# Performance work log

Hardware: AMD Instinct MI355X
Metric: run time of the kernel (lower is better)

Reference implementation:

```python
import jax, jax.numpy as jnp
import numpy as np

HEADS = 8
DIM_HEAD = 64
SCALE = DIM_HEAD ** -0.5
POS_DIM = 64


def _sincos_pe(H, W, dim, dtype):
    # matches build_2d_sincos_pos_embed: [1, dim, H, W]
    y = jnp.linspace(-1.0, 1.0, H)[:, None] * jnp.ones((1, W), jnp.float32)
    x = jnp.ones((H, 1), jnp.float32) * jnp.linspace(-1.0, 1.0, W)[None, :]
    omega = 1.0 / (10000.0 ** (jnp.arange(dim // 4, dtype=jnp.float32) / (dim // 4)))
    px = x[..., None] * omega  # [H, W, dim//4]
    py = y[..., None] * omega
    pe = jnp.concatenate([jnp.sin(px), jnp.cos(px), jnp.sin(py), jnp.cos(py)], axis=-1)
    return pe.transpose(2, 0, 1)[None].astype(dtype)


def _conv2d(x, w):
    return jax.lax.conv_general_dilated(
        x, w, (1, 1), 'SAME', dimension_numbers=('NCHW', 'OIHW', 'NCHW'))


def _sobel(d):
    kx = jnp.array([[1, 0, -1], [2, 0, -2], [1, 0, -1]], jnp.float32).reshape(1, 1, 3, 3)
    ky = jnp.array([[1, 2, 1], [0, 0, 0], [-1, -2, -1]], jnp.float32).reshape(1, 1, 3, 3)
    return _conv2d(d, kx), _conv2d(d, ky)


def setup_inputs() -> dict:
    key = jax.random.key(0)
    ks = jax.random.split(key, 8)
    B, C, H, W = 2, 256, 64, 64
    hid = HEADS * DIM_HEAD  # 512
    s = 0.02
    return {
        'x': jax.random.normal(ks[0], (B, C, H, W), jnp.float32),
        'dsm': jax.random.uniform(ks[1], (B, 1, H, W), jnp.float32),
        'wq': jax.random.normal(ks[2], (hid, C), jnp.float32) * s,
        'wkv': jax.random.normal(ks[3], (2 * hid, C + 1), jnp.float32) * s,
        'wout': jax.random.normal(ks[4], (C, hid), jnp.float32) * s,
        'bout': jnp.zeros((C,), jnp.float32),
        'w_hape': jax.random.normal(ks[5], (hid, POS_DIM + 3), jnp.float32) * s,
        'b_hape': jnp.zeros((hid,), jnp.float32),
        'w_alpha': jax.random.normal(ks[6], (1, 1, 3, 3), jnp.float32) * 0.1,
        'b_alpha': jnp.zeros((1,), jnp.float32),
    }


def reference(x, dsm, wq, wkv, wout, bout, w_hape, b_hape, w_alpha, b_alpha):
    B, C, H, W = x.shape
    hid = wq.shape[0]
    # per-sample min-max normalize DSM over spatial dims
    dmin = dsm.min(axis=(2, 3), keepdims=True)
    dmax = dsm.max(axis=(2, 3), keepdims=True)
    d = (dsm - dmin) / (dmax - dmin + 1e-6)
    # HAPE: [PE | h | grad_h] -> 1x1 conv to hidden
    pe = jnp.broadcast_to(_sincos_pe(H, W, POS_DIM, x.dtype), (B, POS_DIM, H, W))
    gx, gy = _sobel(d)
    hape_in = jnp.concatenate([pe, d, gx, gy], axis=1)  # [B, 67, H, W]
    hape_k = jnp.einsum('oc,bchw->bohw', w_hape, hape_in) + b_hape[None, :, None, None]
    # QKV via 1x1 convs
    q = jnp.einsum('oc,bchw->bohw', wq, x)
    kv = jnp.einsum('oc,bchw->bohw', wkv, jnp.concatenate([x, d], axis=1))
    k = kv[:, :hid] + hape_k
    v = kv[:, hid:]
    to_heads = lambda t: t.reshape(B, HEADS, DIM_HEAD, H * W)  # b (h c) x y -> b h c (xy)
    qh = to_heads(q) * SCALE
    kh = to_heads(k)
    vh = to_heads(v)
    sim = jnp.einsum('bhdi,bhdj->bhij', qh, kh)  # [B, h, N, N]
    attn = jax.nn.softmax(sim, axis=-1)
    out = jnp.einsum('bhij,bhdj->bhid', attn, vh)  # [B, h, N, d]
    # b h (x y) d -> b (h d) x y
    out = out.transpose(0, 1, 3, 2).reshape(B, HEADS * DIM_HEAD, H, W)
    out = jnp.einsum('oc,bchw->bohw', wout, out) + bout[None, :, None, None]
    # fine: gradient-magnitude alpha gating
    mag = jnp.sqrt(jnp.maximum(gx, 0.0) ** 2 + jnp.maximum(gy, 0.0) ** 2 + 1e-12)
    alpha = jax.nn.sigmoid(_conv2d(mag, w_alpha) + b_alpha[None, :, None, None])
    return x + out * alpha
```

## Files before the change

### kernel.cpp

```cpp
#include <hip/hip_runtime.h>
#include <math.h>

#define NPOS 4096
#define MTOT 8192
#define KP   352
#define HT 64
#define WT 64

typedef unsigned short ushortT;
typedef short v8s __attribute__((ext_vector_type(8)));
typedef float v4f __attribute__((ext_vector_type(4)));

static __device__ __forceinline__ ushortT bfr(float f) {
    union { float f; unsigned u; } v; v.f = f;
    return (ushortT)((v.u + 0x8000u) >> 16);
}
static __device__ __forceinline__ unsigned pack2bf(float a, float b) {
    union { float f; unsigned u; } ua, ub; ua.f = a; ub.f = b;
    return __builtin_amdgcn_perm(ub.u + 0x8000u, ua.u + 0x8000u, 0x07060302u);
}
static __device__ __forceinline__ unsigned pack2bf_t(float a, float b) {
    union { float f; unsigned u; } ua, ub; ua.f = a; ub.f = b;
    return __builtin_amdgcn_perm(ub.u, ua.u, 0x07060302u);
}
static __device__ __forceinline__ float fexp2(float x) {
#if __has_builtin(__builtin_amdgcn_exp2f)
    return __builtin_amdgcn_exp2f(x);
#else
    return exp2f(x);
#endif
}

__global__ void k_minmax(const float* __restrict__ dsm, float* __restrict__ mm) {
    int b = blockIdx.x;
    const float* p = dsm + (size_t)b * NPOS;
    float mn = 1e30f, mx = -1e30f;
    for (int i = threadIdx.x; i < NPOS; i += 256) {
        float v = p[i];
        mn = fminf(mn, v); mx = fmaxf(mx, v);
    }
    for (int off = 32; off; off >>= 1) {
        mn = fminf(mn, __shfl_xor(mn, off, 64));
        mx = fmaxf(mx, __shfl_xor(mx, off, 64));
    }
    __shared__ float smn[4], smx[4];
    int wid = threadIdx.x >> 6;
    if ((threadIdx.x & 63) == 0) { smn[wid] = mn; smx[wid] = mx; }
    __syncthreads();
    if (threadIdx.x == 0) {
        mn = fminf(fminf(smn[0], smn[1]), fminf(smn[2], smn[3]));
        mx = fmaxf(fmaxf(smx[0], smx[1]), fmaxf(smx[2], smx[3]));
        mm[b * 2 + 0] = mn; mm[b * 2 + 1] = mx;
    }
}

__global__ void k_prep(const float* __restrict__ dsm, const float* __restrict__ mm,
                       const float* __restrict__ walpha, const float* __restrict__ balpha,
                       ushortT* __restrict__ F, float* __restrict__ alpha) {
    int idx = blockIdx.x * 256 + threadIdx.x;
    int b = idx / NPOS, n = idx % NPOS;
    int hh = n / WT, ww = n % WT;
    float dmin = mm[b * 2], dmax = mm[b * 2 + 1];
    float inv = 1.0f / (dmax - dmin + 1e-6f);
    const float* dp = dsm + (size_t)b * NPOS;

    float dwin[5][5];
    #pragma unroll
    for (int dy = 0; dy < 5; dy++)
        #pragma unroll
        for (int dx = 0; dx < 5; dx++) {
            int y = hh + dy - 2, x = ww + dx - 2;
            float v = 0.0f;
            if (y >= 0 && y < HT && x >= 0 && x < WT) v = (dp[y * WT + x] - dmin) * inv;
            dwin[dy][dx] = v;
        }

    float gxc = 0.f, gyc = 0.f;
    float conv = 0.f;
    #pragma unroll
    for (int oy = 0; oy < 3; oy++)
        #pragma unroll
        for (int ox = 0; ox < 3; ox++) {
            int qy = hh + oy - 1, qx = ww + ox - 1;
            float m = 0.0f;
            if (qy >= 0 && qy < HT && qx >= 0 && qx < WT) {
                float gx = dwin[oy][ox] - dwin[oy][ox + 2]
                         + 2.f * dwin[oy + 1][ox] - 2.f * dwin[oy + 1][ox + 2]
                         + dwin[oy + 2][ox] - dwin[oy + 2][ox + 2];
                float gy = dwin[oy][ox] + 2.f * dwin[oy][ox + 1] + dwin[oy][ox + 2]
                         - dwin[oy + 2][ox] - 2.f * dwin[oy + 2][ox + 1] - dwin[oy + 2][ox + 2];
                if (oy == 1 && ox == 1) { gxc = gx; gyc = gy; }
                float rx = fmaxf(gx, 0.f), ry = fmaxf(gy, 0.f);
                m = sqrtf(rx * rx + ry * ry + 1e-12f);
            }
            conv += walpha[oy * 3 + ox] * m;
        }
    alpha[idx] = 1.f / (1.f + __expf(-(conv + balpha[0])));

    ushortT* fb = F + (size_t)idx * KP;
    fb[256] = bfr(dwin[2][2]);
    fb[257] = bfr(gxc);
    fb[258] = bfr(gyc);
    float xc = -1.f + 2.f * (float)ww / 63.f;
    float yc = -1.f + 2.f * (float)hh / 63.f;
    const float l2w = 13.287712379549449f;
    #pragma unroll
    for (int i = 0; i < 16; i++) {
        float omega = exp2f(-(float)i * (l2w / 16.f));
        float px = xc * omega, py = yc * omega;
        fb[259 + i]      = bfr(__sinf(px));
        fb[259 + 16 + i] = bfr(__cosf(px));
        fb[259 + 32 + i] = bfr(__sinf(py));
        fb[259 + 48 + i] = bfr(__cosf(py));
    }
    #pragma unroll
    for (int z = 323; z < KP; z++) fb[z] = 0;
}

__global__ void k_cast(const float* __restrict__ x, ushortT* __restrict__ F) {
    __shared__ __align__(16) ushortT Tl[64][72];
    int nt = blockIdx.x * 64;
    int b = blockIdx.y >> 2, ct = (blockIdx.y & 3) * 64;
    int t = threadIdx.x;
    #pragma unroll
    for (int rep = 0; rep < 4; rep++) {
        int row = rep * 16 + (t >> 4), c4 = (t & 15) * 4;
        float4 f4 = *(const float4*)&x[((size_t)(b * 256 + ct + row)) * NPOS + nt + c4];
        Tl[c4 + 0][row] = bfr(f4.x);
        Tl[c4 + 1][row] = bfr(f4.y);
        Tl[c4 + 2][row] = bfr(f4.z);
        Tl[c4 + 3][row] = bfr(f4.w);
    }
    __syncthreads();
    #pragma unroll
    for (int rep = 0; rep < 2; rep++) {
        int slot = rep * 256 + t, row = slot >> 3, c8 = slot & 7;
        *(uint4*)&F[((size_t)(b * 4096 + nt + row)) * KP + ct + c8 * 8] = *(uint4*)&Tl[row][c8 * 8];
    }
}

__global__ void k_wcprep(const float* __restrict__ wq, const float* __restrict__ wkv,
                         const float* __restrict__ whape, const float* __restrict__ bhape,
                         ushortT* __restrict__ Wc, float* __restrict__ biasc) {
    int idx = blockIdx.x * 256 + threadIdx.x;
    int o = idx / KP, k = idx % KP;
    float v = 0.f;
    if (o < 512) {
        if (k < 256) v = wq[o * 256 + k] * 0.18033688011112042f;
        if (k == 0) biasc[o] = 0.f;
    } else if (o < 1024) {
        int r = o - 512;
        if (k < 257) v = wkv[r * 257 + k];
        if (k == 256)      v += whape[r * 67 + 64];
        else if (k == 257) v = whape[r * 67 + 65];
        else if (k == 258) v = whape[r * 67 + 66];
        else if (k >= 259 && k < 323) v = whape[r * 67 + (k - 259)];
        if (k == 0) biasc[o] = bhape[r];
    } else {
        int r = o - 512;
        if (k < 257) v = wkv[r * 257 + k];
        if (k == 0) biasc[o] = 0.f;
    }
    Wc[idx] = bfr(v);
}

__global__ void k_wout(const float* __restrict__ wout, ushortT* __restrict__ woutb) {
    int idx = blockIdx.x * 256 + threadIdx.x;
    woutb[idx] = bfr(wout[idx]);
}

__global__ __launch_bounds__(256) void k_gemm1(const ushortT* __restrict__ Wc, const ushortT* __restrict__ F,
                                               const float* __restrict__ biasc,
                                               ushortT* __restrict__ qT, ushortT* __restrict__ kT,
                                               ushortT* __restrict__ vv) {
    __shared__ __align__(16) ushortT Al[64][40];
    __shared__ __align__(16) ushortT Bl[64][40];
    __shared__ __align__(16) ushortT Vt[64][72];
    int mt = blockIdx.x * 64;
    int ot = blockIdx.y * 64;
    int t = threadIdx.x, w = t >> 6, lane = t & 63, u = lane & 15, quad = lane >> 4;
    int arow = t >> 2, ac8 = t & 3;
    v4f acc[4] = {};
    for (int k0 = 0; k0 < KP; k0 += 32) {
        __syncthreads();
        *(uint4*)&Al[arow][ac8 * 8] = *(const uint4*)&Wc[(size_t)(ot + arow) * KP + k0 + ac8 * 8];
        *(uint4*)&Bl[arow][ac8 * 8] = *(const uint4*)&F[(size_t)(mt + arow) * KP + k0 + ac8 * 8];
        __syncthreads();
        v8s a = *(v8s*)&Al[w * 16 + u][quad * 8];
        #pragma unroll
        for (int n4 = 0; n4 < 4; n4++) {
            v8s bb = *(v8s*)&Bl[n4 * 16 + u][quad * 8];
            acc[n4] = __builtin_amdgcn_mfma_f32_16x16x32_bf16(a, bb, acc[n4], 0, 0, 0);
        }
    }
    int obase = ot + w * 16 + quad * 4;
    float bo[4];
    #pragma unroll
    for (int r = 0; r < 4; r++) bo[r] = biasc[obase + r];
    if (ot < 1024) {
        int h = (ot >> 6) & 7;
        ushortT* dst = (ot < 512) ? qT : kT;
        #pragma unroll
        for (int n4 = 0; n4 < 4; n4++) {
            int m = mt + n4 * 16 + u;
            uint2 val;
            val.x = pack2bf(acc[n4][0] + bo[0], acc[n4][1] + bo[1]);
            val.y = pack2bf(acc[n4][2] + bo[2], acc[n4][3] + bo[3]);
            *(uint2*)&dst[((size_t)h * MTOT + m) * 64 + w * 16 + quad * 4] = val;
        }
    } else {
        __syncthreads();
        #pragma unroll
        for (int n4 = 0; n4 < 4; n4++) {
            int ml = n4 * 16 + u;
            #pragma unroll
            for (int r = 0; r < 4; r++) Vt[w * 16 + quad * 4 + r][ml] = bfr(acc[n4][r] + bo[r]);
        }
        __syncthreads();
        #pragma unroll
        for (int rep = 0; rep < 2; rep++) {
            int slot = rep * 256 + t, row = slot >> 3, c8 = slot & 7;
            *(uint4*)&vv[(size_t)(ot - 1024 + row) * MTOT + mt + c8 * 8] = *(uint4*)&Vt[row][c8 * 8];
        }
    }
}

#define LIDX(row, cb) (((row) << 6) + ((((cb) ^ ((row) & 7))) << 3))
__global__ __launch_bounds__(256, 2) void k_flash(const ushortT* __restrict__ qT,
                                                  const ushortT* __restrict__ kT,
                                                  const ushortT* __restrict__ vv,
                                                  float* __restrict__ Opart,
                                                  float* __restrict__ liPart) {
    __shared__ __align__(16) ushortT Kbuf[2][64 * 64];
    __shared__ __align__(16) ushortT Vbuf[2][64 * 64];
    __shared__ __align__(16) ushortT Pw[4][64 * 64];

    int it = blockIdx.x;
    int bh = blockIdx.y;
    int half = blockIdx.z;
    int b = bh >> 3, h = bh & 7;
    int colbase = b * NPOS;
    int t = threadIdx.x, w = t >> 6, lane = t & 63, u = lane & 15, quad = lane >> 4;
    int qb = it * 256 + w * 64;

    const ushortT* Qg = qT + ((size_t)h * MTOT + colbase + qb) * 64;
    const ushortT* Kg = kT + ((size_t)h * MTOT + colbase + half * 2048) * 64;
    const ushortT* Vg = vv + ((size_t)(h * 64)) * MTOT + colbase + half * 2048;
    ushortT* P = &Pw[w][0];

    int row0 = t >> 3,        c80 = t & 7;
    int row1 = (256 + t) >> 3, c81 = t & 7;

    v8s bq[4][2];
    #pragma unroll
    for (int g = 0; g < 4; g++)
        #pragma unroll
        for (int hf = 0; hf < 2; hf++)
            bq[g][hf] = *(const v8s*)&Qg[(size_t)(g * 16 + u) * 64 + hf * 32 + quad * 8];

    float li[4] = {0.f, 0.f, 0.f, 0.f};
    v4f O[4][4] = {};

    uint4 kr0 = *(const uint4*)&Kg[(size_t)row0 * 64 + c80 * 8];
    uint4 kr1 = *(const uint4*)&Kg[(size_t)row1 * 64 + c81 * 8];
    uint4 vr0 = *(const uint4*)&Vg[(size_t)row0 * MTOT + c80 * 8];
    uint4 vr1 = *(const uint4*)&Vg[(size_t)row1 * MTOT + c81 * 8];

    for (int jc = 0; jc < 32; jc++) {
        int cur = jc & 1;
        *(uint4*)&Kbuf[cur][LIDX(row0, c80)] = kr0;
        *(uint4*)&Kbuf[cur][LIDX(row1, c81)] = kr1;
        *(uint4*)&Vbuf[cur][LIDX(row0, c80)] = vr0;
        *(uint4*)&Vbuf[cur][LIDX(row1, c81)] = vr1;
        if (jc + 1 < 32) {
            int jb = (jc + 1) * 64;
            kr0 = *(const uint4*)&Kg[(size_t)(jb + row0) * 64 + c80 * 8];
            kr1 = *(const uint4*)&Kg[(size_t)(jb + row1) * 64 + c81 * 8];
            vr0 = *(const uint4*)&Vg[(size_t)row0 * MTOT + jb + c80 * 8];
            vr1 = *(const uint4*)&Vg[(size_t)row1 * MTOT + jb + c81 * 8];
        }
        __syncthreads();

        const ushortT* Kb = &Kbuf[cur][0];
        const ushortT* Vb = &Vbuf[cur][0];

        #pragma unroll
        for (int k4 = 0; k4 < 4; k4++) {
            v8s ak0 = *(const v8s*)&Kb[LIDX(k4 * 16 + u, quad)];
            v8s ak1 = *(const v8s*)&Kb[LIDX(k4 * 16 + u, 4 + quad)];
            v4f st[4];
            #pragma unroll
            for (int g = 0; g < 4; g++) {
                st[g] = (v4f){0.f, 0.f, 0.f, 0.f};
                st[g] = __builtin_amdgcn_mfma_f32_16x16x32_bf16(ak0, bq[g][0], st[g], 0, 0, 0);
                st[g] = __builtin_amdgcn_mfma_f32_16x16x32_bf16(ak1, bq[g][1], st[g], 0, 0, 0);
            }
            #pragma unroll
            for (int g = 0; g < 4; g++) {
                float p0 = fexp2(st[g][0]);
                float p1 = fexp2(st[g][1]);
                float p2 = fexp2(st[g][2]);
                float p3 = fexp2(st[g][3]);
                li[g] += (p0 + p1) + (p2 + p3);
                uint2 pv; pv.x = pack2bf_t(p0, p1); pv.y = pack2bf_t(p2, p3);
                *(uint2*)&P[LIDX(g * 16 + u, k4 * 2 + (quad >> 1)) + (quad & 1) * 4] = pv;
            }
        }

        v8s bp[4][2];
        #pragma unroll
        for (int g = 0; g < 4; g++)
            #pragma unroll
            for (int ks = 0; ks < 2; ks++)
                bp[g][ks] = *(v8s*)&P[LIDX(g * 16 + u, ks * 4 + quad)];
        #pragma unroll
        for (int d4 = 0; d4 < 4; d4++) {
            v8s av0 = *(const v8s*)&Vb[LIDX(d4 * 16 + u, quad)];
            v8s av1 = *(const v8s*)&Vb[LIDX(d4 * 16 + u, 4 + quad)];
            #pragma unroll
            for (int g = 0; g < 4; g++) {
                O[d4][g] = __builtin_amdgcn_mfma_f32_16x16x32_bf16(av0, bp[g][0], O[d4][g], 0, 0, 0);
                O[d4][g] = __builtin_amdgcn_mfma_f32_16x16x32_bf16(av1, bp[g][1], O[d4][g], 0, 0, 0);
            }
        }
    }

    #pragma unroll
    for (int g = 0; g < 4; g++) {
        li[g] += __shfl_xor(li[g], 16, 64);
        li[g] += __shfl_xor(li[g], 32, 64);
        int q = qb + g * 16 + u;
        size_t m2 = (size_t)(half * 2 + b) * 4096 + q;
        size_t base = m2 * 512 + h * 64;
        #pragma unroll
        for (int d4 = 0; d4 < 4; d4++) {
            float4 o4;
            o4.x = O[d4][g][0]; o4.y = O[d4][g][1]; o4.z = O[d4][g][2]; o4.w = O[d4][g][3];
            *(float4*)&Opart[base + d4 * 16 + quad * 4] = o4;
        }
        if (quad == 0) liPart[m2 * 8 + h] = li[g];
    }
}

__global__ __launch_bounds__(256) void k_comb(const float* __restrict__ Opart,
                                              const float* __restrict__ liPart,
                                              ushortT* __restrict__ aoB) {
    int tid = blockIdx.x * 256 + threadIdx.x;
    int m = tid >> 7, c4 = (tid & 127) * 4, h = c4 >> 6;
    float l = liPart[(size_t)m * 8 + h] + liPart[(size_t)(8192 + m) * 8 + h];
    float inv = 1.f / l;
    float4 o0 = *(const float4*)&Opart[(size_t)m * 512 + c4];
    float4 o1 = *(const float4*)&Opart[(size_t)(8192 + m) * 512 + c4];
    uint2 val;
    val.x = pack2bf((o0.x + o1.x) * inv, (o0.y + o1.y) * inv);
    val.y = pack2bf((o0.z + o1.z) * inv, (o0.w + o1.w) * inv);
    *(uint2*)&aoB[(size_t)m * 512 + c4] = val;
}

__global__ __launch_bounds__(256) void k_gemm2(const ushortT* __restrict__ woutb, const ushortT* __restrict__ aoB,
                                               const float* __restrict__ bout, const float* __restrict__ x,
                                               const float* __restrict__ alpha, float* __restrict__ out) {
    __shared__ __align__(16) ushortT Al[64][40];
    __shared__ __align__(16) ushortT Bl[64][40];
    int mt = blockIdx.x * 64;
    int ot = blockIdx.y * 64;
    int t = threadIdx.x, w = t >> 6, lane = t & 63, u = lane & 15, quad = lane >> 4;
    int arow = t >> 2, ac8 = t & 3;
    v4f acc[4] = {};
    for (int k0 = 0; k0 < 512; k0 += 32) {
        __syncthreads();
        *(uint4*)&Al[arow][ac8 * 8] = *(const uint4*)&woutb[(size_t)(ot + arow) * 512 + k0 + ac8 * 8];
        *(uint4*)&Bl[arow][ac8 * 8] = *(const uint4*)&aoB[(size_t)(mt + arow) * 512 + k0 + ac8 * 8];
        __syncthreads();
        v8s a = *(v8s*)&Al[w * 16 + u][quad * 8];
        #pragma unroll
        for (int n4 = 0; n4 < 4; n4++) {
            v8s bb = *(v8s*)&Bl[n4 * 16 + u][quad * 8];
            acc[n4] = __builtin_amdgcn_mfma_f32_16x16x32_bf16(a, bb, acc[n4], 0, 0, 0);
        }
    }
    int b = mt >> 12, n0 = mt & 4095;
    int obase = ot + w * 16 + quad * 4;
    float bo[4];
    #pragma unroll
    for (int r = 0; r < 4; r++) bo[r] = bout[obase + r];
    #pragma unroll
    for (int n4 = 0; n4 < 4; n4++) {
        int n = n0 + n4 * 16 + u;
        float al = alpha[(size_t)b * NPOS + n];
        #pragma unroll
        for (int r = 0; r < 4; r++) {
            size_t xi = ((size_t)(b * 256 + obase + r)) * NPOS + n;
            out[xi] = x[xi] + (acc[n4][r] + bo[r]) * al;
        }
    }
}

extern "C" void kernel_launch(void* const* d_in, const int* in_sizes, int n_in,
                              void* d_out, int out_size, void* d_ws, size_t ws_size,
                              hipStream_t stream) {
    const float* x      = (const float*)d_in[0];
    const float* dsm    = (const float*)d_in[1];
    const float* wq     = (const float*)d_in[2];
    const float* wkv    = (const float*)d_in[3];
    const float* wout   = (const float*)d_in[4];
    const float* bout   = (const float*)d_in[5];
    const float* whape  = (const float*)d_in[6];
    const float* bhape  = (const float*)d_in[7];
    const float* walpha = (const float*)d_in[8];
    const float* balpha = (const float*)d_in[9];
    float* out = (float*)d_out;
    float* ws  = (float*)d_ws;

    size_t off = 0;
    float* mm    = ws + off; off += 256;
    float* alpha = ws + off; off += (size_t)2 * NPOS;
    float* biasc = ws + off; off += 2048;
    float* Opart  = ws + off; off += (size_t)2 * MTOT * 512;
    float* liPart = ws + off; off += (size_t)2 * MTOT * 8;
    ushortT* F     = (ushortT*)(ws + off); off += (size_t)MTOT * KP / 2;
    ushortT* Wc    = (ushortT*)(ws + off); off += (size_t)1536 * KP / 2;
    ushortT* woutb = (ushortT*)(ws + off); off += (size_t)256 * 512 / 2;
    ushortT* qT    = (ushortT*)(ws + off); off += (size_t)8 * MTOT * 64 / 2;
    ushortT* kT    = (ushortT*)(ws + off); off += (size_t)8 * MTOT * 64 / 2;
    ushortT* vv    = (ushortT*)(ws + off); off += (size_t)512 * MTOT / 2;
    ushortT* aoB   = (ushortT*)(ws + off); off += (size_t)MTOT * 512 / 2;
    (void)in_sizes; (void)n_in; (void)out_size; (void)ws_size;

    k_minmax<<<2, 256, 0, stream>>>(dsm, mm);
    k_prep<<<32, 256, 0, stream>>>(dsm, mm, walpha, balpha, F, alpha);
    k_cast<<<dim3(64, 8), 256, 0, stream>>>(x, F);
    k_wcprep<<<(1536 * KP) / 256, 256, 0, stream>>>(wq, wkv, whape, bhape, Wc, biasc);
    k_wout<<<512, 256, 0, stream>>>(wout, woutb);
    k_gemm1<<<dim3(128, 24), 256, 0, stream>>>(Wc, F, biasc, qT, kT, vv);
    k_flash<<<dim3(16, 16, 2), 256, 0, stream>>>(qT, kT, vv, Opart, liPart);
    k_comb<<<4096, 256, 0, stream>>>(Opart, liPart, aoB);
    k_gemm2<<<dim3(128, 4), 256, 0, stream>>>(woutb, aoB, bout, x, alpha, out);
}
```

Baseline: 212.8 us.

## Use direct global-to-LDS loads in flash, store bf16 partials, fuse combine into gemm2

```diff
diff --git a/kernel.cpp b/kernel.cpp
--- a/kernel.cpp
+++ b/kernel.cpp
@@ -22,6 +22,12 @@
 static __device__ __forceinline__ unsigned pack2bf_t(float a, float b) {
     union { float f; unsigned u; } ua, ub; ua.f = a; ub.f = b;
     return __builtin_amdgcn_perm(ub.u, ua.u, 0x07060302u);
+}
+static __device__ __forceinline__ float bf2f_lo(unsigned v) {
+    union { unsigned u; float f; } x; x.u = v << 16; return x.f;
+}
+static __device__ __forceinline__ float bf2f_hi(unsigned v) {
+    union { unsigned u; float f; } x; x.u = v & 0xffff0000u; return x.f;
 }
 static __device__ __forceinline__ float fexp2(float x) {
 #if __has_builtin(__builtin_amdgcn_exp2f)
@@ -29,6 +35,11 @@
 #else
     return exp2f(x);
 #endif
+}
+static __device__ __forceinline__ void ld_lds16(const ushortT* g, ushortT* l) {
+    __builtin_amdgcn_global_load_lds(
+        (const __attribute__((address_space(1))) unsigned int*)(const void*)g,
+        (__attribute__((address_space(3))) unsigned int*)(void*)l, 16, 0, 0);
 }
 
 __global__ void k_minmax(const float* __restrict__ dsm, float* __restrict__ mm) {
@@ -139,10 +150,18 @@
     }
 }
 
-__global__ void k_wcprep(const float* __restrict__ wq, const float* __restrict__ wkv,
-                         const float* __restrict__ whape, const float* __restrict__ bhape,
-                         ushortT* __restrict__ Wc, float* __restrict__ biasc) {
-    int idx = blockIdx.x * 256 + threadIdx.x;
+__global__ void k_wc(const float* __restrict__ wq, const float* __restrict__ wkv,
+                     const float* __restrict__ whape, const float* __restrict__ bhape,
+                     const float* __restrict__ wout,
+                     ushortT* __restrict__ Wc, float* __restrict__ biasc,
+                     ushortT* __restrict__ woutb) {
+    int bid = blockIdx.x;
+    if (bid >= 2112) {
+        int idx = (bid - 2112) * 256 + threadIdx.x;
+        woutb[idx] = bfr(wout[idx]);
+        return;
+    }
+    int idx = bid * 256 + threadIdx.x;
     int o = idx / KP, k = idx % KP;
     float v = 0.f;
     if (o < 512) {
@@ -164,11 +183,6 @@
     Wc[idx] = bfr(v);
 }
 
-__global__ void k_wout(const float* __restrict__ wout, ushortT* __restrict__ woutb) {
-    int idx = blockIdx.x * 256 + threadIdx.x;
-    woutb[idx] = bfr(wout[idx]);
-}
-
 __global__ __launch_bounds__(256) void k_gemm1(const ushortT* __restrict__ Wc, const ushortT* __restrict__ F,
                                                const float* __restrict__ biasc,
                                                ushortT* __restrict__ qT, ushortT* __restrict__ kT,
@@ -225,15 +239,15 @@
     }
 }
 
-#define LIDX(row, cb) (((row) << 6) + ((((cb) ^ ((row) & 7))) << 3))
+#define FRAG(f) ((f) * 512)
 __global__ __launch_bounds__(256, 2) void k_flash(const ushortT* __restrict__ qT,
                                                   const ushortT* __restrict__ kT,
                                                   const ushortT* __restrict__ vv,
-                                                  float* __restrict__ Opart,
+                                                  ushortT* __restrict__ OpB,
                                                   float* __restrict__ liPart) {
-    __shared__ __align__(16) ushortT Kbuf[2][64 * 64];
-    __shared__ __align__(16) ushortT Vbuf[2][64 * 64];
-    __shared__ __align__(16) ushortT Pw[4][64 * 64];
+    __shared__ __align__(16) ushortT Kbuf[2][8 * 512];
+    __shared__ __align__(16) ushortT Vbuf[2][8 * 512];
+    __shared__ __align__(16) ushortT Pw[4][8 * 512];
 
     int it = blockIdx.x;
     int bh = blockIdx.y;
@@ -248,9 +262,6 @@
     const ushortT* Vg = vv + ((size_t)(h * 64)) * MTOT + colbase + half * 2048;
     ushortT* P = &Pw[w][0];
 
-    int row0 = t >> 3,        c80 = t & 7;
-    int row1 = (256 + t) >> 3, c81 = t & 7;
-
     v8s bq[4][2];
     #pragma unroll
     for (int g = 0; g < 4; g++)
@@ -261,33 +272,26 @@
     float li[4] = {0.f, 0.f, 0.f, 0.f};
     v4f O[4][4] = {};
 
-    uint4 kr0 = *(const uint4*)&Kg[(size_t)row0 * 64 + c80 * 8];
-    uint4 kr1 = *(const uint4*)&Kg[(size_t)row1 * 64 + c81 * 8];
-    uint4 vr0 = *(const uint4*)&Vg[(size_t)row0 * MTOT + c80 * 8];
-    uint4 vr1 = *(const uint4*)&Vg[(size_t)row1 * MTOT + c81 * 8];
+    auto stage = [&](int jb, int bufi) {
+        ld_lds16(&Kg[(size_t)(jb + w * 16 + u) * 64 + 0 * 32 + quad * 8], &Kbuf[bufi][FRAG(2 * w + 0)]);
+        ld_lds16(&Kg[(size_t)(jb + w * 16 + u) * 64 + 1 * 32 + quad * 8], &Kbuf[bufi][FRAG(2 * w + 1)]);
+        ld_lds16(&Vg[(size_t)(w * 16 + u) * MTOT + jb + 0 * 32 + quad * 8], &Vbuf[bufi][FRAG(2 * w + 0)]);
+        ld_lds16(&Vg[(size_t)(w * 16 + u) * MTOT + jb + 1 * 32 + quad * 8], &Vbuf[bufi][FRAG(2 * w + 1)]);
+    };
+
+    stage(0, 0);
+    __syncthreads();
 
     for (int jc = 0; jc < 32; jc++) {
         int cur = jc & 1;
-        *(uint4*)&Kbuf[cur][LIDX(row0, c80)] = kr0;
-        *(uint4*)&Kbuf[cur][LIDX(row1, c81)] = kr1;
-        *(uint4*)&Vbuf[cur][LIDX(row0, c80)] = vr0;
-        *(uint4*)&Vbuf[cur][LIDX(row1, c81)] = vr1;
-        if (jc + 1 < 32) {
-            int jb = (jc + 1) * 64;
-            kr0 = *(const uint4*)&Kg[(size_t)(jb + row0) * 64 + c80 * 8];
-            kr1 = *(const uint4*)&Kg[(size_t)(jb + row1) * 64 + c81 * 8];
-            vr0 = *(const uint4*)&Vg[(size_t)row0 * MTOT + jb + c80 * 8];
-            vr1 = *(const uint4*)&Vg[(size_t)row1 * MTOT + jb + c81 * 8];
-        }
-        __syncthreads();
-
+        if (jc + 1 < 32) stage((jc + 1) * 64, cur ^ 1);
         const ushortT* Kb = &Kbuf[cur][0];
         const ushortT* Vb = &Vbuf[cur][0];
 
         #pragma unroll
         for (int k4 = 0; k4 < 4; k4++) {
-            v8s ak0 = *(const v8s*)&Kb[LIDX(k4 * 16 + u, quad)];
-            v8s ak1 = *(const v8s*)&Kb[LIDX(k4 * 16 + u, 4 + quad)];
+            v8s ak0 = *(const v8s*)&Kb[FRAG(k4 * 2 + 0) + lane * 8];
+            v8s ak1 = *(const v8s*)&Kb[FRAG(k4 * 2 + 1) + lane * 8];
             v4f st[4];
             #pragma unroll
             for (int g = 0; g < 4; g++) {
@@ -303,7 +307,8 @@
                 float p3 = fexp2(st[g][3]);
                 li[g] += (p0 + p1) + (p2 + p3);
                 uint2 pv; pv.x = pack2bf_t(p0, p1); pv.y = pack2bf_t(p2, p3);
-                *(uint2*)&P[LIDX(g * 16 + u, k4 * 2 + (quad >> 1)) + (quad & 1) * 4] = pv;
+                *(uint2*)&P[FRAG(g * 2 + (k4 >> 1)) +
+                            ((((k4 & 1) * 2 + (quad >> 1)) * 16 + u) * 8) + (quad & 1) * 4] = pv;
             }
         }
 
@@ -312,52 +317,39 @@
         for (int g = 0; g < 4; g++)
             #pragma unroll
             for (int ks = 0; ks < 2; ks++)
-                bp[g][ks] = *(v8s*)&P[LIDX(g * 16 + u, ks * 4 + quad)];
+                bp[g][ks] = *(v8s*)&P[FRAG(g * 2 + ks) + lane * 8];
         #pragma unroll
         for (int d4 = 0; d4 < 4; d4++) {
-            v8s av0 = *(const v8s*)&Vb[LIDX(d4 * 16 + u, quad)];
-            v8s av1 = *(const v8s*)&Vb[LIDX(d4 * 16 + u, 4 + quad)];
+            v8s av0 = *(const v8s*)&Vb[FRAG(d4 * 2 + 0) + lane * 8];
+            v8s av1 = *(const v8s*)&Vb[FRAG(d4 * 2 + 1) + lane * 8];
             #pragma unroll
             for (int g = 0; g < 4; g++) {
                 O[d4][g] = __builtin_amdgcn_mfma_f32_16x16x32_bf16(av0, bp[g][0], O[d4][g], 0, 0, 0);
                 O[d4][g] = __builtin_amdgcn_mfma_f32_16x16x32_bf16(av1, bp[g][1], O[d4][g], 0, 0, 0);
             }
         }
+        __syncthreads();
     }
 
     #pragma unroll
     for (int g = 0; g < 4; g++) {
         li[g] += __shfl_xor(li[g], 16, 64);
         li[g] += __shfl_xor(li[g], 32, 64);
-        int q = qb + g * 16 + u;
-        size_t m2 = (size_t)(half * 2 + b) * 4096 + q;
+        size_t m2 = (size_t)(half * 2 + b) * 4096 + qb + g * 16 + u;
         size_t base = m2 * 512 + h * 64;
         #pragma unroll
         for (int d4 = 0; d4 < 4; d4++) {
-            float4 o4;
-            o4.x = O[d4][g][0]; o4.y = O[d4][g][1]; o4.z = O[d4][g][2]; o4.w = O[d4][g][3];
-            *(float4*)&Opart[base + d4 * 16 + quad * 4] = o4;
+            uint2 val;
+            val.x = pack2bf(O[d4][g][0], O[d4][g][1]);
+            val.y = pack2bf(O[d4][g][2], O[d4][g][3]);
+            *(uint2*)&OpB[base + d4 * 16 + quad * 4] = val;
         }
         if (quad == 0) liPart[m2 * 8 + h] = li[g];
     }
 }
 
-__global__ __launch_bounds__(256) void k_comb(const float* __restrict__ Opart,
-                                              const float* __restrict__ liPart,
-                                              ushortT* __restrict__ aoB) {
-    int tid = blockIdx.x * 256 + threadIdx.x;
-    int m = tid >> 7, c4 = (tid & 127) * 4, h = c4 >> 6;
-    float l = liPart[(size_t)m * 8 + h] + liPart[(size_t)(8192 + m) * 8 + h];
-    float inv = 1.f / l;
-    float4 o0 = *(const float4*)&Opart[(size_t)m * 512 + c4];
-    float4 o1 = *(const float4*)&Opart[(size_t)(8192 + m) * 512 + c4];
-    uint2 val;
-    val.x = pack2bf((o0.x + o1.x) * inv, (o0.y + o1.y) * inv);
-    val.y = pack2bf((o0.z + o1.z) * inv, (o0.w + o1.w) * inv);
-    *(uint2*)&aoB[(size_t)m * 512 + c4] = val;
-}
-
-__global__ __launch_bounds__(256) void k_gemm2(const ushortT* __restrict__ woutb, const ushortT* __restrict__ aoB,
+__global__ __launch_bounds__(256) void k_gemm2(const ushortT* __restrict__ woutb, const ushortT* __restrict__ OpB,
+                                               const float* __restrict__ liPart,
                                                const float* __restrict__ bout, const float* __restrict__ x,
                                                const float* __restrict__ alpha, float* __restrict__ out) {
     __shared__ __align__(16) ushortT Al[64][40];
@@ -366,11 +358,25 @@
     int ot = blockIdx.y * 64;
     int t = threadIdx.x, w = t >> 6, lane = t & 63, u = lane & 15, quad = lane >> 4;
     int arow = t >> 2, ac8 = t & 3;
+    int mg = mt + arow;
     v4f acc[4] = {};
     for (int k0 = 0; k0 < 512; k0 += 32) {
         __syncthreads();
         *(uint4*)&Al[arow][ac8 * 8] = *(const uint4*)&woutb[(size_t)(ot + arow) * 512 + k0 + ac8 * 8];
-        *(uint4*)&Bl[arow][ac8 * 8] = *(const uint4*)&aoB[(size_t)(mt + arow) * 512 + k0 + ac8 * 8];
+        {
+            int col = k0 + ac8 * 8;
+            int hh = col >> 6;
+            float l = liPart[(size_t)mg * 8 + hh] + liPart[(size_t)(8192 + mg) * 8 + hh];
+            float inv = 1.f / l;
+            uint4 o0 = *(const uint4*)&OpB[(size_t)mg * 512 + col];
+            uint4 o1 = *(const uint4*)&OpB[(size_t)(8192 + mg) * 512 + col];
+            uint4 r;
+            r.x = pack2bf((bf2f_lo(o0.x) + bf2f_lo(o1.x)) * inv, (bf2f_hi(o0.x) + bf2f_hi(o1.x)) * inv);
+            r.y = pack2bf((bf2f_lo(o0.y) + bf2f_lo(o1.y)) * inv, (bf2f_hi(o0.y) + bf2f_hi(o1.y)) * inv);
+            r.z = pack2bf((bf2f_lo(o0.z) + bf2f_lo(o1.z)) * inv, (bf2f_hi(o0.z) + bf2f_hi(o1.z)) * inv);
+            r.w = pack2bf((bf2f_lo(o0.w) + bf2f_lo(o1.w)) * inv, (bf2f_hi(o0.w) + bf2f_hi(o1.w)) * inv);
+            *(uint4*)&Bl[arow][ac8 * 8] = r;
+        }
         __syncthreads();
         v8s a = *(v8s*)&Al[w * 16 + u][quad * 8];
         #pragma unroll
@@ -413,27 +419,24 @@
     float* ws  = (float*)d_ws;
 
     size_t off = 0;
-    float* mm    = ws + off; off += 256;
-    float* alpha = ws + off; off += (size_t)2 * NPOS;
-    float* biasc = ws + off; off += 2048;
-    float* Opart  = ws + off; off += (size_t)2 * MTOT * 512;
+    float* mm     = ws + off; off += 256;
+    float* alpha  = ws + off; off += (size_t)2 * NPOS;
+    float* biasc  = ws + off; off += 2048;
     float* liPart = ws + off; off += (size_t)2 * MTOT * 8;
+    ushortT* OpB   = (ushortT*)(ws + off); off += (size_t)2 * MTOT * 512 / 2;
     ushortT* F     = (ushortT*)(ws + off); off += (size_t)MTOT * KP / 2;
     ushortT* Wc    = (ushortT*)(ws + off); off += (size_t)1536 * KP / 2;
     ushortT* woutb = (ushortT*)(ws + off); off += (size_t)256 * 512 / 2;
     ushortT* qT    = (ushortT*)(ws + off); off += (size_t)8 * MTOT * 64 / 2;
     ushortT* kT    = (ushortT*)(ws + off); off += (size_t)8 * MTOT * 64 / 2;
     ushortT* vv    = (ushortT*)(ws + off); off += (size_t)512 * MTOT / 2;
-    ushortT* aoB   = (ushortT*)(ws + off); off += (size_t)MTOT * 512 / 2;
     (void)in_sizes; (void)n_in; (void)out_size; (void)ws_size;
 
     k_minmax<<<2, 256, 0, stream>>>(dsm, mm);
     k_prep<<<32, 256, 0, stream>>>(dsm, mm, walpha, balpha, F, alpha);
     k_cast<<<dim3(64, 8), 256, 0, stream>>>(x, F);
-    k_wcprep<<<(1536 * KP) / 256, 256, 0, stream>>>(wq, wkv, whape, bhape, Wc, biasc);
-    k_wout<<<512, 256, 0, stream>>>(wout, woutb);
+    k_wc<<<2624, 256, 0, stream>>>(wq, wkv, whape, bhape, wout, Wc, biasc, woutb);
     k_gemm1<<<dim3(128, 24), 256, 0, stream>>>(Wc, F, biasc, qT, kT, vv);
-    k_flash<<<dim3(16, 16, 2), 256, 0, stream>>>(qT, kT, vv, Opart, liPart);
-    k_comb<<<4096, 256, 0, stream>>>(Opart, liPart, aoB);
-    k_gemm2<<<dim3(128, 4), 256, 0, stream>>>(woutb, aoB, bout, x, alpha, out);
-}
+    k_flash<<<dim3(16, 16, 2), 256, 0, stream>>>(qT, kT, vv, OpB, liPart);
+    k_gemm2<<<dim3(128, 4), 256, 0, stream>>>(woutb, OpB, liPart, bout, x, alpha, out);
+}
```

Result: slower. 221.1 us (+3.9%).
